# Kernel tuning notes

Hardware: AMD Instinct MI355X
Metric: run time of the kernel (lower is better)

Reference implementation:

```python
import jax, jax.numpy as jnp
import numpy as np

N_NODES = 50000
N_EDGES = 800000
N_HIDDEN = 64
N_LAYER = 3
IN_DIM = 4


def setup_inputs() -> dict:
    key = jax.random.key(0)
    ks = jax.random.split(key, 10)
    x = jax.random.normal(ks[0], (N_NODES, IN_DIM), dtype=jnp.float32)
    edge_index = jax.random.randint(ks[1], (2, N_EDGES), 0, N_NODES, dtype=jnp.int64)
    # Glorot-style params matching pyg GCNConv (lin has no bias; conv adds bias after aggregation)
    def glorot(k, fan_in, fan_out):
        s = jnp.sqrt(6.0 / (fan_in + fan_out))
        return jax.random.uniform(k, (fan_in, fan_out), jnp.float32, -s, s)
    W_in = glorot(ks[2], IN_DIM, N_HIDDEN)
    b_in = jnp.zeros((N_HIDDEN,), jnp.float32)
    W_h = jnp.stack([glorot(jax.random.fold_in(ks[3], i), N_HIDDEN, N_HIDDEN) for i in range(N_LAYER)])
    b_h = jnp.zeros((N_LAYER, N_HIDDEN), jnp.float32)
    W_out = glorot(ks[4], N_HIDDEN, 1)
    b_out = jnp.zeros((1,), jnp.float32)
    return {"x": x, "edge_index": edge_index, "W_in": W_in, "b_in": b_in,
            "W_h": W_h, "b_h": b_h, "W_out": W_out, "b_out": b_out}


def _gcn_norm(edge_index, n_nodes):
    # add self-loops, compute symmetric norm D^{-1/2} (A+I) D^{-1/2}
    loop = jnp.arange(n_nodes, dtype=edge_index.dtype)
    src = jnp.concatenate([edge_index[0], loop])
    dst = jnp.concatenate([edge_index[1], loop])
    deg = jax.ops.segment_sum(jnp.ones_like(dst, dtype=jnp.float32), dst, num_segments=n_nodes)
    dinv = jax.lax.rsqrt(deg)  # deg >= 1 due to self-loops
    norm = dinv[src] * dinv[dst]
    return src, dst, norm


def _gcn_conv(x, W, b, src, dst, norm, n_nodes):
    h = x @ W                                   # [N, out]
    msg = h[src] * norm[:, None]                # gather + scale, [E+N, out]
    out = jax.ops.segment_sum(msg, dst, num_segments=n_nodes)  # scatter-add
    return out + b


def reference(x, edge_index, W_in, b_in, W_h, b_h, W_out, b_out):
    n = x.shape[0]
    src, dst, norm = _gcn_norm(edge_index, n)
    h = jax.nn.relu(_gcn_conv(x, W_in, b_in, src, dst, norm, n))
    for i in range(W_h.shape[0]):
        h = jax.nn.relu(_gcn_conv(h, W_h[i], b_h[i], src, dst, norm, n))
    return _gcn_conv(h, W_out, b_out, src, dst, norm, n)
```

## Files before the change

kernel.cpp:

```cpp
#include <hip/hip_runtime.h>
#include <hip/hip_bf16.h>


#define TPB 256
#define EPT 8
#define CHUNK (TPB * EPT)
typedef __hip_bfloat16 bf16;
#define B2F __bfloat162float

__global__ void k_zero_b(int* __restrict__ bktcnt, int* __restrict__ ticket) {
    bktcnt[threadIdx.x] = 0;
    if (threadIdx.x == 0) *ticket = 0;
}

__global__ __launch_bounds__(TPB) void k_bktcnt(
    const int* __restrict__ dst, int* __restrict__ bktcnt, int* __restrict__ ticket,
    int* __restrict__ bktbase, int* __restrict__ bcur, int E, int n) {
    __shared__ int h[256];
    __shared__ int lastFlag;
    int tid = threadIdx.x;
    h[tid] = 0;
    __syncthreads();
    int e0 = blockIdx.x * CHUNK;
#pragma unroll
    for (int u = 0; u < EPT; ++u) {
        int e = e0 + u * TPB + tid;
        if (e < E) {
            int d = dst[e];
            if ((unsigned)d < (unsigned)n) atomicAdd(&h[d >> 8], 1);
        }
    }
    __syncthreads();
    if (h[tid]) atomicAdd(&bktcnt[tid], h[tid]);
    __threadfence();
    __syncthreads();
    if (tid == 0) lastFlag = (atomicAdd(ticket, 1) == (int)gridDim.x - 1);
    __syncthreads();
    if (!lastFlag) return;
    int v = atomicAdd(&bktcnt[tid], 0);
    h[tid] = v;
    __syncthreads();
    for (int off = 1; off < 256; off <<= 1) {
        int u2 = (tid >= off) ? h[tid - off] : 0;
        __syncthreads();
        h[tid] += u2;
        __syncthreads();
    }
    int excl = h[tid] - v;
    bktbase[tid] = excl;
    bcur[tid] = excl;
    if (tid == 255) bktbase[256] = h[tid];
}

__global__ __launch_bounds__(TPB) void k_bin(
    const int* __restrict__ src, const int* __restrict__ dst,
    int* __restrict__ bcur, unsigned* __restrict__ staging, int E, int n) {
    __shared__ int hcnt[256];
    __shared__ int hbase[256];
    int tid = threadIdx.x;
    int e0 = blockIdx.x * CHUNK;
    hcnt[tid] = 0;
    __syncthreads();

    int eb[EPT];
    unsigned rec[EPT];
#pragma unroll
    for (int u = 0; u < EPT; ++u) {
        int e = e0 + u * TPB + tid;
        eb[u] = -1;
        if (e < E) {
            int d = dst[e], s = src[e];
            if ((unsigned)d < (unsigned)n && (unsigned)s < (unsigned)n) {
                eb[u] = d >> 8;
                rec[u] = (unsigned)s | ((unsigned)(d & 255) << 16);
                atomicAdd(&hcnt[eb[u]], 1);
            }
        }
    }
    __syncthreads();
    int c = hcnt[tid];
    hbase[tid] = (c > 0) ? atomicAdd(&bcur[tid], c) : 0;
    hcnt[tid] = 0;
    __syncthreads();
#pragma unroll
    for (int u = 0; u < EPT; ++u) {
        if (eb[u] >= 0) {
            int r = atomicAdd(&hcnt[eb[u]], 1);
            int pos = hbase[eb[u]] + r;
            if ((unsigned)pos < (unsigned)E) staging[pos] = rec[u];
        }
    }
}

__global__ __launch_bounds__(TPB) void k_unbin2(
    const unsigned* __restrict__ staging, const int* __restrict__ bktbase,
    int* __restrict__ row_start, float* __restrict__ dinv,
    unsigned short* __restrict__ bucket, int E, int n) {
    __shared__ int cnt[256];
    __shared__ int scn[256];
    __shared__ int cur[256];
    int b = blockIdx.x, tid = threadIdx.x;
    int lo = bktbase[b], hi = bktbase[b + 1];
    lo = max(0, min(lo, E)); hi = max(lo, min(hi, E));

    cnt[tid] = 0;
    __syncthreads();
    for (int i = lo + tid; i < hi; i += TPB)
        atomicAdd(&cnt[(staging[i] >> 16) & 255], 1);
    __syncthreads();

    int v = cnt[tid];
    scn[tid] = v;
    __syncthreads();
    for (int off = 1; off < 256; off <<= 1) {
        int u = (tid >= off) ? scn[tid - off] : 0;
        __syncthreads();
        scn[tid] += u;
        __syncthreads();
    }
    int excl = scn[tid] - v;
    int base = min(lo + excl, E);
    cur[tid] = base;
    int d = (b << 8) + tid;
    if (d < n) {
        row_start[d] = base;
        dinv[d] = rsqrtf((float)v + 1.0f);
        if (d == n - 1) row_start[n] = min(base + v, E);
    }
    __syncthreads();

    for (int i = lo + tid; i < hi; i += TPB) {
        unsigned r = staging[i];
        int t = (r >> 16) & 255;
        int pos = atomicAdd(&cur[t], 1);
        if ((unsigned)pos < (unsigned)E) bucket[pos] = (unsigned short)(r & 0xffffu);
    }
}

__global__ void k_mm_in(const float* __restrict__ x, const float* __restrict__ W,
                        const float* __restrict__ dinv, bf16* __restrict__ g, int n) {
    int t = blockIdx.x * blockDim.x + threadIdx.x;
    if (t >= n * 64) return;
    int i = t >> 6, j = t & 63;
    float acc = 0.f;
#pragma unroll
    for (int k = 0; k < 4; ++k) acc = fmaf(x[i * 4 + k], W[k * 64 + j], acc);
    g[t] = __float2bfloat16(acc * dinv[i]);
}

__device__ __forceinline__ void acc_oct(float* a, uint4 w) {
    a[0] += __uint_as_float(w.x << 16);
    a[1] += __uint_as_float(w.x & 0xffff0000u);
    a[2] += __uint_as_float(w.y << 16);
    a[3] += __uint_as_float(w.y & 0xffff0000u);
    a[4] += __uint_as_float(w.z << 16);
    a[5] += __uint_as_float(w.z & 0xffff0000u);
    a[6] += __uint_as_float(w.w << 16);
    a[7] += __uint_as_float(w.w & 0xffff0000u);
}

__device__ __forceinline__ void agg_oct(const bf16* __restrict__ g,
                                        const unsigned short* __restrict__ bucket,
                                        int k0, int k1, int d, float* __restrict__ a,
                                        int lane, unsigned nm1, unsigned Em1) {
    int grp = lane >> 3, i = lane & 7;
#pragma unroll
    for (int m = 0; m < 8; ++m) a[m] = 0.f;
    if (grp == 0) {
        uint4 w = *(const uint4*)(g + (size_t)d * 64 + 8 * i);
        acc_oct(a, w);
    }
    for (int base = k0; base < k1; base += 64) {
        int cnt = min(64, k1 - base);
        int rec = bucket[min((unsigned)(base + lane), Em1)];
        int k = 0;
        for (; k + 16 <= cnt; k += 16) {
            unsigned s0 = min((unsigned)__shfl(rec, k + grp), nm1);
            unsigned s1 = min((unsigned)__shfl(rec, k + 8 + grp), nm1);
            uint4 w0 = *(const uint4*)(g + (size_t)s0 * 64 + 8 * i);
            uint4 w1 = *(const uint4*)(g + (size_t)s1 * 64 + 8 * i);
            acc_oct(a, w0);
            acc_oct(a, w1);
        }
        for (; k < cnt; k += 8) {
            int e = k + grp;
            unsigned s = min((unsigned)__shfl(rec, min(e, 63)), nm1);
            uint4 w = *(const uint4*)(g + (size_t)s * 64 + 8 * i);
            if (e < cnt) acc_oct(a, w);
        }
    }
}

__global__ __launch_bounds__(TPB) void k_gconv(
    const bf16* __restrict__ gIn, const float* __restrict__ dinv,
    const int* __restrict__ row_start, const unsigned short* __restrict__ bucket,
    const float* __restrict__ bias, const float* __restrict__ W,
    bf16* __restrict__ gOut, int n, int E) {
    __shared__ float sW[4096];
    __shared__ float sAct[4][64];
    int tid = threadIdx.x;
    const float4* W4 = (const float4*)W;
    float4* sW4 = (float4*)sW;
#pragma unroll
    for (int t = 0; t < 4; ++t) sW4[tid + t * 256] = W4[tid + t * 256];
    __syncthreads();

    int r = tid >> 6, j = tid & 63;
    int grp = j >> 3, i = j & 7;
    int d0 = blockIdx.x * 8 + r * 2;
    if (d0 >= n) return;
    unsigned nm1 = (unsigned)(n - 1), Em1 = (unsigned)(E - 1);

    for (int q = 0; q < 2; ++q) {
        int d = d0 + q;
        if (d >= n) break;
        float dd = dinv[d];
        int k0 = row_start[d], k1 = row_start[d + 1];
        k1 = min(k1, E); k0 = max(min(k0, k1), 0);
        float a[8];
        agg_oct(gIn, bucket, k0, k1, d, a, j, nm1, Em1);
#pragma unroll
        for (int m = 0; m < 8; ++m) {
            a[m] += __shfl_xor(a[m], 8);
            a[m] += __shfl_xor(a[m], 16);
            a[m] += __shfl_xor(a[m], 32);
        }
        if (grp == 0) {
            const float4* b4 = (const float4*)bias;
            float4 bA = b4[2 * i], bB = b4[2 * i + 1];
            float4 r0, r1;
            r0.x = fmaxf(fmaf(dd, a[0], bA.x), 0.f);
            r0.y = fmaxf(fmaf(dd, a[1], bA.y), 0.f);
            r0.z = fmaxf(fmaf(dd, a[2], bA.z), 0.f);
            r0.w = fmaxf(fmaf(dd, a[3], bA.w), 0.f);
            r1.x = fmaxf(fmaf(dd, a[4], bB.x), 0.f);
            r1.y = fmaxf(fmaf(dd, a[5], bB.y), 0.f);
            r1.z = fmaxf(fmaf(dd, a[6], bB.z), 0.f);
            r1.w = fmaxf(fmaf(dd, a[7], bB.w), 0.f);
            float4* arow = (float4*)&sAct[r][8 * i];
            arow[0] = r0; arow[1] = r1;
        }
        const float4* ap = (const float4*)&sAct[r][0];
        float acc0 = 0.f, acc1 = 0.f, acc2 = 0.f, acc3 = 0.f;
#pragma unroll
        for (int k4 = 0; k4 < 16; ++k4) {
            float4 a4 = ap[k4];
            acc0 = fmaf(a4.x, sW[(4 * k4 + 0) * 64 + j], acc0);
            acc1 = fmaf(a4.y, sW[(4 * k4 + 1) * 64 + j], acc1);
            acc2 = fmaf(a4.z, sW[(4 * k4 + 2) * 64 + j], acc2);
            acc3 = fmaf(a4.w, sW[(4 * k4 + 3) * 64 + j], acc3);
        }
        float acc = (acc0 + acc1) + (acc2 + acc3);
        gOut[(size_t)d * 64 + j] = __float2bfloat16(acc * dd);
    }
}

__global__ __launch_bounds__(TPB) void k_gconv_z(
    const bf16* __restrict__ gIn, const float* __restrict__ dinv,
    const int* __restrict__ row_start, const unsigned short* __restrict__ bucket,
    const float* __restrict__ bias, const float* __restrict__ Wout,
    float* __restrict__ zg, int n, int E) {
    int tid = threadIdx.x;
    int r = tid >> 6, j = tid & 63;
    int d = blockIdx.x * 4 + r;
    if (d >= n) return;
    float dd = dinv[d];
    int k0 = row_start[d], k1 = row_start[d + 1];
    k1 = min(k1, E); k0 = max(min(k0, k1), 0);
    float a[8];
    agg_oct(gIn, bucket, k0, k1, d, a, j, (unsigned)(n - 1), (unsigned)(E - 1));
#pragma unroll
    for (int m = 0; m < 8; ++m) {
        a[m] += __shfl_xor(a[m], 8);
        a[m] += __shfl_xor(a[m], 16);
        a[m] += __shfl_xor(a[m], 32);
    }
    int i = j & 7;
    const float4* b4 = (const float4*)bias;
    const float4* w4 = (const float4*)Wout;
    float4 bA = b4[2 * i], bB = b4[2 * i + 1];
    float4 wA = w4[2 * i], wB = w4[2 * i + 1];
    float p = fmaxf(fmaf(dd, a[0], bA.x), 0.f) * wA.x
            + fmaxf(fmaf(dd, a[1], bA.y), 0.f) * wA.y
            + fmaxf(fmaf(dd, a[2], bA.z), 0.f) * wA.z
            + fmaxf(fmaf(dd, a[3], bA.w), 0.f) * wA.w
            + fmaxf(fmaf(dd, a[4], bB.x), 0.f) * wB.x
            + fmaxf(fmaf(dd, a[5], bB.y), 0.f) * wB.y
            + fmaxf(fmaf(dd, a[6], bB.z), 0.f) * wB.z
            + fmaxf(fmaf(dd, a[7], bB.w), 0.f) * wB.w;
    p += __shfl_xor(p, 1);
    p += __shfl_xor(p, 2);
    p += __shfl_xor(p, 4);
    if (j == 0) zg[d] = p * dd;
}

__global__ __launch_bounds__(TPB) void k_out(
    const float* __restrict__ zg, const float* __restrict__ dinv,
    const int* __restrict__ row_start, const unsigned short* __restrict__ bucket,
    const float* __restrict__ b_out, float* __restrict__ out, int n, int E) {
    int t = blockIdx.x * blockDim.x + threadIdx.x;
    int d = t >> 6, lane = t & 63;
    if (d >= n) return;
    int k0 = row_start[d], k1 = row_start[d + 1];
    k1 = min(k1, E); k0 = max(min(k0, k1), 0);
    unsigned nm1 = (unsigned)(n - 1);
    float v = 0.f;
    for (int k = k0 + lane; k < k1; k += 64) {
        unsigned s = min((unsigned)bucket[k], nm1);
        v += zg[s];
    }
#pragma unroll
    for (int off = 32; off > 0; off >>= 1) v += __shfl_down(v, off);
    if (lane == 0) out[d] = fmaf(zg[d] + v, dinv[d], b_out[0]);
}

extern "C" void kernel_launch(void* const* d_in, const int* in_sizes, int n_in,
                              void* d_out, int out_size, void* d_ws, size_t ws_size,
                              hipStream_t stream) {
    const float* x     = (const float*)d_in[0];
    const int*   ei    = (const int*)d_in[1];
    const float* W_in  = (const float*)d_in[2];
    const float* b_in  = (const float*)d_in[3];
    const float* W_h   = (const float*)d_in[4];
    const float* b_h   = (const float*)d_in[5];
    const float* W_out = (const float*)d_in[6];
    const float* b_out = (const float*)d_in[7];
    float* out = (float*)d_out;

    int N = in_sizes[0] / 4;
    int E = in_sizes[1] / 2;
    const int* src = ei;
    const int* dst = ei + E;

    char* ws = (char*)d_ws;
    bf16* gA               = (bf16*)ws;           ws += (size_t)N * 64 * 2;
    bf16* gB               = (bf16*)ws;           ws += (size_t)N * 64 * 2;
    unsigned short* bucket = (unsigned short*)ws; ws += (size_t)E * 2;
    unsigned* staging      = (unsigned*)ws;       ws += (size_t)E * 4;
    int*  row_start        = (int*)ws;            ws += (size_t)(N + 1) * 4;
    float* dinv            = (float*)ws;          ws += (size_t)N * 4;
    float* zg              = (float*)ws;          ws += (size_t)N * 4;
    int*  bktcnt           = (int*)ws;            ws += 256 * 4;
    int*  ticket           = (int*)ws;            ws += 4;
    int*  bktbase          = (int*)ws;            ws += 257 * 4;
    int*  bcur             = (int*)ws;

    int B   = (N + 255) >> 8;
    int gNF = (N * 64 + TPB - 1) / TPB;
    int gN4 = (N + 3) / 4;
    int gN8 = (N + 7) / 8;
    int gBin = (E + CHUNK - 1) / CHUNK;

    k_zero_b<<<1, 256, 0, stream>>>(bktcnt, ticket);
    k_bktcnt<<<gBin, TPB, 0, stream>>>(dst, bktcnt, ticket, bktbase, bcur, E, N);
    k_bin<<<gBin, TPB, 0, stream>>>(src, dst, bcur, staging, E, N);
    k_unbin2<<<B, TPB, 0, stream>>>(staging, bktbase, row_start, dinv, bucket, E, N);

    k_mm_in<<<gNF, TPB, 0, stream>>>(x, W_in, dinv, gA, N);
    k_gconv<<<gN8, TPB, 0, stream>>>(gA, dinv, row_start, bucket, b_in, W_h, gB, N, E);
    k_gconv<<<gN8, TPB, 0, stream>>>(gB, dinv, row_start, bucket, b_h, W_h + 4096, gA, N, E);
    k_gconv<<<gN8, TPB, 0, stream>>>(gA, dinv, row_start, bucket, b_h + 64, W_h + 8192, gB, N, E);
    k_gconv_z<<<gN4, TPB, 0, stream>>>(gB, dinv, row_start, bucket, b_h + 128, W_out, zg, N, E);
    k_out<<<gN4, TPB, 0, stream>>>(zg, dinv, row_start, bucket, b_out, out, N, E);
}
```

Before: 322.1 us.

## Assign one 8-lane group per destination node and batch 8 nodes per wave

Restructures the aggregation so each 8-lane subgroup handles a whole destination node, instead of a full 64-lane wave cooperating on one node. This removes the cross-group shuffle reductions and the idle lanes on low-degree nodes (average degree about 17). The dense 64x64 transform now runs over 8 nodes per wave from shared memory, so each weight load is reused 8 times. The cost is load imbalance within a wave when node degrees differ, and more registers for the eight accumulators.

```diff
diff --git a/kernel.cpp b/kernel.cpp
--- a/kernel.cpp
+++ b/kernel.cpp
@@ -159,34 +159,24 @@
     a[7] += __uint_as_float(w.w & 0xffff0000u);
 }
 
-__device__ __forceinline__ void agg_oct(const bf16* __restrict__ g,
+__device__ __forceinline__ void agg_grp(const bf16* __restrict__ g,
                                         const unsigned short* __restrict__ bucket,
-                                        int k0, int k1, int d, float* __restrict__ a,
-                                        int lane, unsigned nm1, unsigned Em1) {
-    int grp = lane >> 3, i = lane & 7;
+                                        int k0, int k1, int dc, float* __restrict__ a,
+                                        int i, unsigned nm1, unsigned Em1) {
 #pragma unroll
     for (int m = 0; m < 8; ++m) a[m] = 0.f;
-    if (grp == 0) {
-        uint4 w = *(const uint4*)(g + (size_t)d * 64 + 8 * i);
+    {
+        uint4 w = *(const uint4*)(g + (size_t)dc * 64 + 8 * i);
         acc_oct(a, w);
     }
-    for (int base = k0; base < k1; base += 64) {
-        int cnt = min(64, k1 - base);
-        int rec = bucket[min((unsigned)(base + lane), Em1)];
-        int k = 0;
-        for (; k + 16 <= cnt; k += 16) {
-            unsigned s0 = min((unsigned)__shfl(rec, k + grp), nm1);
-            unsigned s1 = min((unsigned)__shfl(rec, k + 8 + grp), nm1);
-            uint4 w0 = *(const uint4*)(g + (size_t)s0 * 64 + 8 * i);
-            uint4 w1 = *(const uint4*)(g + (size_t)s1 * 64 + 8 * i);
-            acc_oct(a, w0);
-            acc_oct(a, w1);
-        }
-        for (; k < cnt; k += 8) {
-            int e = k + grp;
-            unsigned s = min((unsigned)__shfl(rec, min(e, 63)), nm1);
+    for (int t0 = k0; t0 < k1; t0 += 8) {
+        int rec = bucket[min((unsigned)(t0 + i), Em1)];
+        int m = k1 - t0;
+#pragma unroll
+        for (int e = 0; e < 8; ++e) {
+            unsigned s = min((unsigned)__shfl(rec, e, 8), nm1);
             uint4 w = *(const uint4*)(g + (size_t)s * 64 + 8 * i);
-            if (e < cnt) acc_oct(a, w);
+            if (e < m) acc_oct(a, w);
         }
     }
 }
@@ -197,7 +187,7 @@
     const float* __restrict__ bias, const float* __restrict__ W,
     bf16* __restrict__ gOut, int n, int E) {
     __shared__ float sW[4096];
-    __shared__ float sAct[4][64];
+    __shared__ float sAct[4][8][68];
     int tid = threadIdx.x;
     const float4* W4 = (const float4*)W;
     float4* sW4 = (float4*)sW;
@@ -207,51 +197,54 @@
 
     int r = tid >> 6, j = tid & 63;
     int grp = j >> 3, i = j & 7;
-    int d0 = blockIdx.x * 8 + r * 2;
-    if (d0 >= n) return;
+    int base = (blockIdx.x * 4 + r) * 8;
+    if (base >= n) return;
     unsigned nm1 = (unsigned)(n - 1), Em1 = (unsigned)(E - 1);
-
-    for (int q = 0; q < 2; ++q) {
-        int d = d0 + q;
-        if (d >= n) break;
-        float dd = dinv[d];
-        int k0 = row_start[d], k1 = row_start[d + 1];
-        k1 = min(k1, E); k0 = max(min(k0, k1), 0);
-        float a[8];
-        agg_oct(gIn, bucket, k0, k1, d, a, j, nm1, Em1);
-#pragma unroll
-        for (int m = 0; m < 8; ++m) {
-            a[m] += __shfl_xor(a[m], 8);
-            a[m] += __shfl_xor(a[m], 16);
-            a[m] += __shfl_xor(a[m], 32);
-        }
-        if (grp == 0) {
-            const float4* b4 = (const float4*)bias;
-            float4 bA = b4[2 * i], bB = b4[2 * i + 1];
-            float4 r0, r1;
-            r0.x = fmaxf(fmaf(dd, a[0], bA.x), 0.f);
-            r0.y = fmaxf(fmaf(dd, a[1], bA.y), 0.f);
-            r0.z = fmaxf(fmaf(dd, a[2], bA.z), 0.f);
-            r0.w = fmaxf(fmaf(dd, a[3], bA.w), 0.f);
-            r1.x = fmaxf(fmaf(dd, a[4], bB.x), 0.f);
-            r1.y = fmaxf(fmaf(dd, a[5], bB.y), 0.f);
-            r1.z = fmaxf(fmaf(dd, a[6], bB.z), 0.f);
-            r1.w = fmaxf(fmaf(dd, a[7], bB.w), 0.f);
-            float4* arow = (float4*)&sAct[r][8 * i];
-            arow[0] = r0; arow[1] = r1;
-        }
-        const float4* ap = (const float4*)&sAct[r][0];
-        float acc0 = 0.f, acc1 = 0.f, acc2 = 0.f, acc3 = 0.f;
-#pragma unroll
-        for (int k4 = 0; k4 < 16; ++k4) {
-            float4 a4 = ap[k4];
-            acc0 = fmaf(a4.x, sW[(4 * k4 + 0) * 64 + j], acc0);
-            acc1 = fmaf(a4.y, sW[(4 * k4 + 1) * 64 + j], acc1);
-            acc2 = fmaf(a4.z, sW[(4 * k4 + 2) * 64 + j], acc2);
-            acc3 = fmaf(a4.w, sW[(4 * k4 + 3) * 64 + j], acc3);
-        }
-        float acc = (acc0 + acc1) + (acc2 + acc3);
-        gOut[(size_t)d * 64 + j] = __float2bfloat16(acc * dd);
+    int d = base + grp;
+    int dc = min(d, n - 1);
+    float dd = dinv[dc];
+    int k0 = row_start[dc], k1 = row_start[dc + 1];
+    k1 = min(k1, E); k0 = max(min(k0, k1), 0);
+    if (d >= n) k1 = k0;
+
+    float a[8];
+    agg_grp(gIn, bucket, k0, k1, dc, a, i, nm1, Em1);
+
+    const float4* b4 = (const float4*)bias;
+    float4 bA = b4[2 * i], bB = b4[2 * i + 1];
+    float4 r0, r1;
+    r0.x = fmaxf(fmaf(dd, a[0], bA.x), 0.f);
+    r0.y = fmaxf(fmaf(dd, a[1], bA.y), 0.f);
+    r0.z = fmaxf(fmaf(dd, a[2], bA.z), 0.f);
+    r0.w = fmaxf(fmaf(dd, a[3], bA.w), 0.f);
+    r1.x = fmaxf(fmaf(dd, a[4], bB.x), 0.f);
+    r1.y = fmaxf(fmaf(dd, a[5], bB.y), 0.f);
+    r1.z = fmaxf(fmaf(dd, a[6], bB.z), 0.f);
+    r1.w = fmaxf(fmaf(dd, a[7], bB.w), 0.f);
+    float4* arow = (float4*)&sAct[r][grp][8 * i];
+    arow[0] = r0; arow[1] = r1;
+
+    float acc[8] = {0.f, 0.f, 0.f, 0.f, 0.f, 0.f, 0.f, 0.f};
+#pragma unroll
+    for (int k4 = 0; k4 < 16; ++k4) {
+        float w0 = sW[(4 * k4 + 0) * 64 + j];
+        float w1 = sW[(4 * k4 + 1) * 64 + j];
+        float w2 = sW[(4 * k4 + 2) * 64 + j];
+        float w3 = sW[(4 * k4 + 3) * 64 + j];
+#pragma unroll
+        for (int g = 0; g < 8; ++g) {
+            float4 av = *(const float4*)&sAct[r][g][4 * k4];
+            acc[g] = fmaf(av.x, w0, acc[g]);
+            acc[g] = fmaf(av.y, w1, acc[g]);
+            acc[g] = fmaf(av.z, w2, acc[g]);
+            acc[g] = fmaf(av.w, w3, acc[g]);
+        }
+    }
+#pragma unroll
+    for (int g = 0; g < 8; ++g) {
+        float ddg = __shfl(dd, g * 8);
+        if (base + g < n)
+            gOut[(size_t)(base + g) * 64 + j] = __float2bfloat16(acc[g] * ddg);
     }
 }
 
@@ -262,20 +255,20 @@
     float* __restrict__ zg, int n, int E) {
     int tid = threadIdx.x;
     int r = tid >> 6, j = tid & 63;
-    int d = blockIdx.x * 4 + r;
-    if (d >= n) return;
-    float dd = dinv[d];
-    int k0 = row_start[d], k1 = row_start[d + 1];
+    int grp = j >> 3, i = j & 7;
+    int base = (blockIdx.x * 4 + r) * 8;
+    if (base >= n) return;
+    unsigned nm1 = (unsigned)(n - 1), Em1 = (unsigned)(E - 1);
+    int d = base + grp;
+    int dc = min(d, n - 1);
+    float dd = dinv[dc];
+    int k0 = row_start[dc], k1 = row_start[dc + 1];
     k1 = min(k1, E); k0 = max(min(k0, k1), 0);
+    if (d >= n) k1 = k0;
+
     float a[8];
-    agg_oct(gIn, bucket, k0, k1, d, a, j, (unsigned)(n - 1), (unsigned)(E - 1));
-#pragma unroll
-    for (int m = 0; m < 8; ++m) {
-        a[m] += __shfl_xor(a[m], 8);
-        a[m] += __shfl_xor(a[m], 16);
-        a[m] += __shfl_xor(a[m], 32);
-    }
-    int i = j & 7;
+    agg_grp(gIn, bucket, k0, k1, dc, a, i, nm1, Em1);
+
     const float4* b4 = (const float4*)bias;
     const float4* w4 = (const float4*)Wout;
     float4 bA = b4[2 * i], bB = b4[2 * i + 1];
@@ -288,30 +281,34 @@
             + fmaxf(fmaf(dd, a[5], bB.y), 0.f) * wB.y
             + fmaxf(fmaf(dd, a[6], bB.z), 0.f) * wB.z
             + fmaxf(fmaf(dd, a[7], bB.w), 0.f) * wB.w;
-    p += __shfl_xor(p, 1);
-    p += __shfl_xor(p, 2);
-    p += __shfl_xor(p, 4);
-    if (j == 0) zg[d] = p * dd;
+    p += __shfl_xor(p, 1, 8);
+    p += __shfl_xor(p, 2, 8);
+    p += __shfl_xor(p, 4, 8);
+    if (i == 0 && d < n) zg[d] = p * dd;
 }
 
 __global__ __launch_bounds__(TPB) void k_out(
     const float* __restrict__ zg, const float* __restrict__ dinv,
     const int* __restrict__ row_start, const unsigned short* __restrict__ bucket,
     const float* __restrict__ b_out, float* __restrict__ out, int n, int E) {
-    int t = blockIdx.x * blockDim.x + threadIdx.x;
-    int d = t >> 6, lane = t & 63;
-    if (d >= n) return;
-    int k0 = row_start[d], k1 = row_start[d + 1];
+    int tid = threadIdx.x;
+    int r = tid >> 6, j = tid & 63;
+    int grp = j >> 3, i = j & 7;
+    int base = (blockIdx.x * 4 + r) * 8;
+    if (base >= n) return;
+    int d = base + grp;
+    int dc = min(d, n - 1);
+    int k0 = row_start[dc], k1 = row_start[dc + 1];
     k1 = min(k1, E); k0 = max(min(k0, k1), 0);
+    if (d >= n) k1 = k0;
     unsigned nm1 = (unsigned)(n - 1);
     float v = 0.f;
-    for (int k = k0 + lane; k < k1; k += 64) {
-        unsigned s = min((unsigned)bucket[k], nm1);
-        v += zg[s];
-    }
-#pragma unroll
-    for (int off = 32; off > 0; off >>= 1) v += __shfl_down(v, off);
-    if (lane == 0) out[d] = fmaf(zg[d] + v, dinv[d], b_out[0]);
+    for (int k = k0 + i; k < k1; k += 8)
+        v += zg[min((unsigned)bucket[k], nm1)];
+    v += __shfl_xor(v, 1, 8);
+    v += __shfl_xor(v, 2, 8);
+    v += __shfl_xor(v, 4, 8);
+    if (i == 0 && d < n) out[d] = fmaf(zg[d] + v, dinv[d], b_out[0]);
 }
 
 extern "C" void kernel_launch(void* const* d_in, const int* in_sizes, int n_in,
@@ -345,10 +342,9 @@
     int*  bktbase          = (int*)ws;            ws += 257 * 4;
     int*  bcur             = (int*)ws;
 
-    int B   = (N + 255) >> 8;
-    int gNF = (N * 64 + TPB - 1) / TPB;
-    int gN4 = (N + 3) / 4;
-    int gN8 = (N + 7) / 8;
+    int B    = (N + 255) >> 8;
+    int gNF  = (N * 64 + TPB - 1) / TPB;
+    int gN32 = (N + 31) / 32;
     int gBin = (E + CHUNK - 1) / CHUNK;
 
     k_zero_b<<<1, 256, 0, stream>>>(bktcnt, ticket);
@@ -357,9 +353,9 @@
     k_unbin2<<<B, TPB, 0, stream>>>(staging, bktbase, row_start, dinv, bucket, E, N);
 
     k_mm_in<<<gNF, TPB, 0, stream>>>(x, W_in, dinv, gA, N);
-    k_gconv<<<gN8, TPB, 0, stream>>>(gA, dinv, row_start, bucket, b_in, W_h, gB, N, E);
-    k_gconv<<<gN8, TPB, 0, stream>>>(gB, dinv, row_start, bucket, b_h, W_h + 4096, gA, N, E);
-    k_gconv<<<gN8, TPB, 0, stream>>>(gA, dinv, row_start, bucket, b_h + 64, W_h + 8192, gB, N, E);
-    k_gconv_z<<<gN4, TPB, 0, stream>>>(gB, dinv, row_start, bucket, b_h + 128, W_out, zg, N, E);
-    k_out<<<gN4, TPB, 0, stream>>>(zg, dinv, row_start, bucket, b_out, out, N, E);
-}
+    k_gconv<<<gN32, TPB, 0, stream>>>(gA, dinv, row_start, bucket, b_in, W_h, gB, N, E);
+    k_gconv<<<gN32, TPB, 0, stream>>>(gB, dinv, row_start, bucket, b_h, W_h + 4096, gA, N, E);
+    k_gconv<<<gN32, TPB, 0, stream>>>(gA, dinv, row_start, bucket, b_h + 64, W_h + 8192, gB, N, E);
+    k_gconv_z<<<gN32, TPB, 0, stream>>>(gB, dinv, row_start, bucket, b_h + 128, W_out, zg, N, E);
+    k_out<<<gN32, TPB, 0, stream>>>(zg, dinv, row_start, bucket, b_out, out, N, E);
+}
```

Measured after the change: 433.2 us. +34.5%, slower.

## Use persistent gconv blocks with register-held weights and LDS partial reduction

Applied to the files above, without the earlier changes.

The hidden GCN layer kernel now runs as a persistent grid of 1024 blocks that stride over nodes, one wavefront per node. Each lane keeps its column of W in registers, loaded once, instead of staging the 16KB weight matrix in shared memory in every block. The cross-lane shuffle reduction of the eight edge-group partials is replaced by a padded shared-memory transpose and sum, and the final kernel likewise uses one feature per lane with a shuffle-down reduction. The 64 weight registers per lane raise register pressure, and the shared-memory reduction has no explicit barriers, so it relies on wavefront lockstep within each row.

```diff
diff --git a/kernel.cpp b/kernel.cpp
--- a/kernel.cpp
+++ b/kernel.cpp
@@ -191,64 +191,49 @@
     }
 }
 
-__global__ __launch_bounds__(TPB) void k_gconv(
+__global__ __launch_bounds__(TPB, 4) void k_gconv(
     const bf16* __restrict__ gIn, const float* __restrict__ dinv,
     const int* __restrict__ row_start, const unsigned short* __restrict__ bucket,
     const float* __restrict__ bias, const float* __restrict__ W,
     bf16* __restrict__ gOut, int n, int E) {
-    __shared__ float sW[4096];
-    __shared__ float sAct[4][64];
+    __shared__ float sVp[4][8][68];
     int tid = threadIdx.x;
-    const float4* W4 = (const float4*)W;
-    float4* sW4 = (float4*)sW;
-#pragma unroll
-    for (int t = 0; t < 4; ++t) sW4[tid + t * 256] = W4[tid + t * 256];
-    __syncthreads();
-
     int r = tid >> 6, j = tid & 63;
     int grp = j >> 3, i = j & 7;
-    int d0 = blockIdx.x * 8 + r * 2;
-    if (d0 >= n) return;
     unsigned nm1 = (unsigned)(n - 1), Em1 = (unsigned)(E - 1);
 
-    for (int q = 0; q < 2; ++q) {
-        int d = d0 + q;
-        if (d >= n) break;
+    float wreg[64];
+#pragma unroll
+    for (int k = 0; k < 64; ++k) wreg[k] = W[k * 64 + j];
+    float bj = bias[j];
+
+    int nw = gridDim.x * 4;
+    for (int d = blockIdx.x * 4 + r; d < n; d += nw) {
         float dd = dinv[d];
         int k0 = row_start[d], k1 = row_start[d + 1];
         k1 = min(k1, E); k0 = max(min(k0, k1), 0);
+
         float a[8];
         agg_oct(gIn, bucket, k0, k1, d, a, j, nm1, Em1);
-#pragma unroll
-        for (int m = 0; m < 8; ++m) {
-            a[m] += __shfl_xor(a[m], 8);
-            a[m] += __shfl_xor(a[m], 16);
-            a[m] += __shfl_xor(a[m], 32);
-        }
-        if (grp == 0) {
-            const float4* b4 = (const float4*)bias;
-            float4 bA = b4[2 * i], bB = b4[2 * i + 1];
-            float4 r0, r1;
-            r0.x = fmaxf(fmaf(dd, a[0], bA.x), 0.f);
-            r0.y = fmaxf(fmaf(dd, a[1], bA.y), 0.f);
-            r0.z = fmaxf(fmaf(dd, a[2], bA.z), 0.f);
-            r0.w = fmaxf(fmaf(dd, a[3], bA.w), 0.f);
-            r1.x = fmaxf(fmaf(dd, a[4], bB.x), 0.f);
-            r1.y = fmaxf(fmaf(dd, a[5], bB.y), 0.f);
-            r1.z = fmaxf(fmaf(dd, a[6], bB.z), 0.f);
-            r1.w = fmaxf(fmaf(dd, a[7], bB.w), 0.f);
-            float4* arow = (float4*)&sAct[r][8 * i];
-            arow[0] = r0; arow[1] = r1;
-        }
-        const float4* ap = (const float4*)&sAct[r][0];
+
+        float4* prow = (float4*)&sVp[r][grp][8 * i];
+        prow[0] = make_float4(a[0], a[1], a[2], a[3]);
+        prow[1] = make_float4(a[4], a[5], a[6], a[7]);
+        float full = 0.f;
+#pragma unroll
+        for (int g = 0; g < 8; ++g) full += sVp[r][g][j];
+
+        float act = fmaxf(fmaf(dd, full, bj), 0.f);
+        sVp[r][0][j] = act;
+
         float acc0 = 0.f, acc1 = 0.f, acc2 = 0.f, acc3 = 0.f;
 #pragma unroll
         for (int k4 = 0; k4 < 16; ++k4) {
-            float4 a4 = ap[k4];
-            acc0 = fmaf(a4.x, sW[(4 * k4 + 0) * 64 + j], acc0);
-            acc1 = fmaf(a4.y, sW[(4 * k4 + 1) * 64 + j], acc1);
-            acc2 = fmaf(a4.z, sW[(4 * k4 + 2) * 64 + j], acc2);
-            acc3 = fmaf(a4.w, sW[(4 * k4 + 3) * 64 + j], acc3);
+            float4 av = *(const float4*)&sVp[r][0][4 * k4];
+            acc0 = fmaf(av.x, wreg[4 * k4 + 0], acc0);
+            acc1 = fmaf(av.y, wreg[4 * k4 + 1], acc1);
+            acc2 = fmaf(av.z, wreg[4 * k4 + 2], acc2);
+            acc3 = fmaf(av.w, wreg[4 * k4 + 3], acc3);
         }
         float acc = (acc0 + acc1) + (acc2 + acc3);
         gOut[(size_t)d * 64 + j] = __float2bfloat16(acc * dd);
@@ -260,37 +245,29 @@
     const int* __restrict__ row_start, const unsigned short* __restrict__ bucket,
     const float* __restrict__ bias, const float* __restrict__ Wout,
     float* __restrict__ zg, int n, int E) {
+    __shared__ float sVp[4][8][68];
     int tid = threadIdx.x;
     int r = tid >> 6, j = tid & 63;
+    int grp = j >> 3, i = j & 7;
     int d = blockIdx.x * 4 + r;
     if (d >= n) return;
     float dd = dinv[d];
     int k0 = row_start[d], k1 = row_start[d + 1];
     k1 = min(k1, E); k0 = max(min(k0, k1), 0);
+
     float a[8];
     agg_oct(gIn, bucket, k0, k1, d, a, j, (unsigned)(n - 1), (unsigned)(E - 1));
-#pragma unroll
-    for (int m = 0; m < 8; ++m) {
-        a[m] += __shfl_xor(a[m], 8);
-        a[m] += __shfl_xor(a[m], 16);
-        a[m] += __shfl_xor(a[m], 32);
-    }
-    int i = j & 7;
-    const float4* b4 = (const float4*)bias;
-    const float4* w4 = (const float4*)Wout;
-    float4 bA = b4[2 * i], bB = b4[2 * i + 1];
-    float4 wA = w4[2 * i], wB = w4[2 * i + 1];
-    float p = fmaxf(fmaf(dd, a[0], bA.x), 0.f) * wA.x
-            + fmaxf(fmaf(dd, a[1], bA.y), 0.f) * wA.y
-            + fmaxf(fmaf(dd, a[2], bA.z), 0.f) * wA.z
-            + fmaxf(fmaf(dd, a[3], bA.w), 0.f) * wA.w
-            + fmaxf(fmaf(dd, a[4], bB.x), 0.f) * wB.x
-            + fmaxf(fmaf(dd, a[5], bB.y), 0.f) * wB.y
-            + fmaxf(fmaf(dd, a[6], bB.z), 0.f) * wB.z
-            + fmaxf(fmaf(dd, a[7], bB.w), 0.f) * wB.w;
-    p += __shfl_xor(p, 1);
-    p += __shfl_xor(p, 2);
-    p += __shfl_xor(p, 4);
+
+    float4* prow = (float4*)&sVp[r][grp][8 * i];
+    prow[0] = make_float4(a[0], a[1], a[2], a[3]);
+    prow[1] = make_float4(a[4], a[5], a[6], a[7]);
+    float full = 0.f;
+#pragma unroll
+    for (int g = 0; g < 8; ++g) full += sVp[r][g][j];
+
+    float p = fmaxf(fmaf(dd, full, bias[j]), 0.f) * Wout[j];
+#pragma unroll
+    for (int off = 32; off > 0; off >>= 1) p += __shfl_down(p, off);
     if (j == 0) zg[d] = p * dd;
 }
 
@@ -345,11 +322,11 @@
     int*  bktbase          = (int*)ws;            ws += 257 * 4;
     int*  bcur             = (int*)ws;
 
-    int B   = (N + 255) >> 8;
-    int gNF = (N * 64 + TPB - 1) / TPB;
-    int gN4 = (N + 3) / 4;
-    int gN8 = (N + 7) / 8;
-    int gBin = (E + CHUNK - 1) / CHUNK;
+    int B     = (N + 255) >> 8;
+    int gNF   = (N * 64 + TPB - 1) / TPB;
+    int gN4   = (N + 3) / 4;
+    int gPers = 1024;
+    int gBin  = (E + CHUNK - 1) / CHUNK;
 
     k_zero_b<<<1, 256, 0, stream>>>(bktcnt, ticket);
     k_bktcnt<<<gBin, TPB, 0, stream>>>(dst, bktcnt, ticket, bktbase, bcur, E, N);
@@ -357,9 +334,9 @@
     k_unbin2<<<B, TPB, 0, stream>>>(staging, bktbase, row_start, dinv, bucket, E, N);
 
     k_mm_in<<<gNF, TPB, 0, stream>>>(x, W_in, dinv, gA, N);
-    k_gconv<<<gN8, TPB, 0, stream>>>(gA, dinv, row_start, bucket, b_in, W_h, gB, N, E);
-    k_gconv<<<gN8, TPB, 0, stream>>>(gB, dinv, row_start, bucket, b_h, W_h + 4096, gA, N, E);
-    k_gconv<<<gN8, TPB, 0, stream>>>(gA, dinv, row_start, bucket, b_h + 64, W_h + 8192, gB, N, E);
+    k_gconv<<<gPers, TPB, 0, stream>>>(gA, dinv, row_start, bucket, b_in, W_h, gB, N, E);
+    k_gconv<<<gPers, TPB, 0, stream>>>(gB, dinv, row_start, bucket, b_h, W_h + 4096, gA, N, E);
+    k_gconv<<<gPers, TPB, 0, stream>>>(gA, dinv, row_start, bucket, b_h + 64, W_h + 8192, gB, N, E);
     k_gconv_z<<<gN4, TPB, 0, stream>>>(gB, dinv, row_start, bucket, b_h + 128, W_out, zg, N, E);
     k_out<<<gN4, TPB, 0, stream>>>(zg, dinv, row_start, bucket, b_out, out, N, E);
 }
```

Result: faster. 270.7 us (-16.0%).
